# Performance work log

Hardware: AMD Instinct MI355X
Metric: run time of the kernel (lower is better)

## Reference

```python
import jax, jax.numpy as jnp
import numpy as np


def _l2norm(x, axis=-1, eps=1e-12):
    # matches F.normalize(p=2): x / max(||x||, eps)
    n = jnp.sqrt(jnp.sum(x * x, axis=axis, keepdims=True))
    return x / jnp.maximum(n, eps)


def setup_inputs() -> dict:
    key = jax.random.key(0)
    k1, k2 = jax.random.split(key)
    B, D, C = 262144, 256, 1000
    features = jax.random.normal(k1, (B, D), dtype=jnp.float32)
    labels = jax.random.randint(k2, (B,), 0, C, dtype=jnp.int64)
    return {"features": features, "labels": labels, "num_classes": C}


def reference(features, labels, num_classes):
    labels = labels.astype(jnp.int32)
    f = _l2norm(features, axis=1)  # (B, D)
    # per-class scatter-mean (classes with zero samples contribute no loss terms)
    sums = jax.ops.segment_sum(f, labels, num_segments=num_classes)      # (C, D)
    counts = jax.ops.segment_sum(jnp.ones((f.shape[0],), f.dtype), labels,
                                 num_segments=num_classes)               # (C,)
    protos = sums / jnp.maximum(counts, 1.0)[:, None]
    protos = _l2norm(protos, axis=1)                                     # (C, D)
    # cosine distance of each sample to its own class prototype
    p = protos[labels]                                                   # (B, D)
    dist = 1.0 - jnp.sum(f * p, axis=1)                                  # (B,)
    B = f.shape[0]
    return jnp.sum(dist) / jnp.maximum(B, 1)
```

## Files before the change

kernel.cpp:

```cpp
#include <hip/hip_runtime.h>


#define DIM 256
#define NB 64
#define SSB 2048

typedef float fx4 __attribute__((ext_vector_type(4)));

__global__ __launch_bounds__(256) void k_hist(const int* __restrict__ labels,
                                              int* __restrict__ hist,
                                              float* __restrict__ sums,
                                              int B, int C) {
  extern __shared__ int s_h[];
  const int tid = threadIdx.x;
  for (int i = blockIdx.x * 256 + tid; i < C * DIM; i += NB * 256)
    sums[i] = 0.f;
  for (int c = tid; c < C; c += 256) s_h[c] = 0;
  __syncthreads();
  const int chunk = (B + NB - 1) / NB;
  const int r0 = blockIdx.x * chunk;
  const int r1 = min(B, r0 + chunk);
  for (int i = r0 + tid; i < r1; i += 256) atomicAdd(&s_h[labels[i]], 1);
  __syncthreads();
  int* dst = hist + (size_t)blockIdx.x * C;
  for (int c = tid; c < C; c += 256) dst[c] = s_h[c];
}

__global__ __launch_bounds__(1024) void k_scan(int* __restrict__ hist,
                                               float* __restrict__ out, int C) {
  __shared__ int s[2][1024];
  const int tid = threadIdx.x;
  if (tid == 0) out[0] = 0.f;
  int total = 0;
  if (tid < C) {
    int run = 0;
    for (int b = 0; b < NB; ++b) {
      int* p = hist + (size_t)b * C + tid;
      const int h = *p;
      *p = run;
      run += h;
    }
    total = run;
  }
  int cur = 0;
  s[0][tid] = total;
  __syncthreads();
  for (int d = 1; d < 1024; d <<= 1) {
    const int v = s[cur][tid] + (tid >= d ? s[cur][tid - d] : 0);
    s[1 - cur][tid] = v;
    __syncthreads();
    cur ^= 1;
  }
  const int exoff = s[cur][tid] - total;
  if (tid < C)
    for (int b = 0; b < NB; ++b) hist[(size_t)b * C + tid] += exoff;
}

__global__ __launch_bounds__(256) void k_permute(const int* __restrict__ labels,
                                                 const int* __restrict__ bases,
                                                 int2* __restrict__ pr,
                                                 int B, int C) {
  extern __shared__ int s_cur[];
  const int tid = threadIdx.x;
  const int* bp = bases + (size_t)blockIdx.x * C;
  for (int c = tid; c < C; c += 256) s_cur[c] = bp[c];
  __syncthreads();
  const int chunk = (B + NB - 1) / NB;
  const int r0 = blockIdx.x * chunk;
  const int r1 = min(B, r0 + chunk);
  for (int i = r0 + tid; i < r1; i += 256) {
    const int l = labels[i];
    const int pos = atomicAdd(&s_cur[l], 1);
    pr[pos] = make_int2(i, l);
  }
}

__device__ __forceinline__ void flush_acc(float* __restrict__ sums, int c,
                                          const fx4& a, int lane) {
  float* dst = sums + (size_t)c * DIM + lane * 4;
  atomicAdd(dst + 0, a.x);
  atomicAdd(dst + 1, a.y);
  atomicAdd(dst + 2, a.z);
  atomicAdd(dst + 3, a.w);
}

__global__ __launch_bounds__(256) void k_segsum(const float* __restrict__ x,
                                                const int2* __restrict__ pr,
                                                float* __restrict__ sums,
                                                int B) {
  const int lane = threadIdx.x & 63;
  const int wid = __builtin_amdgcn_readfirstlane(
      (blockIdx.x << 2) | (threadIdx.x >> 6));
  const int nw = SSB * 4;
  const int per = (B + nw - 1) / nw;
  const int r0 = wid * per;
  const int r1 = min(B, r0 + per);
  if (r0 >= r1) return;

  fx4 acc = {0.f, 0.f, 0.f, 0.f};
  int prev = -1;
  int rb = r0;

  for (; rb + 8 <= r1; rb += 8) {
    int2 e[8];
#pragma unroll
    for (int k = 0; k < 8; ++k) e[k] = pr[rb + k];
    fx4 v[8];
#pragma unroll
    for (int k = 0; k < 8; ++k)
      v[k] = __builtin_nontemporal_load(
          (const fx4*)(x + (size_t)e[k].x * DIM) + lane);
    float ss[8];
#pragma unroll
    for (int k = 0; k < 8; ++k)
      ss[k] = v[k].x * v[k].x + v[k].y * v[k].y + v[k].z * v[k].z +
              v[k].w * v[k].w;
#pragma unroll
    for (int off = 32; off; off >>= 1) {
#pragma unroll
      for (int k = 0; k < 8; ++k) ss[k] += __shfl_xor(ss[k], off);
    }
#pragma unroll
    for (int k = 0; k < 8; ++k) {
      const float inv = 1.f / fmaxf(sqrtf(ss[k]), 1e-12f);
      const int lab = e[k].y;
      if (lab != prev) {
        if (prev >= 0) flush_acc(sums, prev, acc, lane);
        acc = (fx4){0.f, 0.f, 0.f, 0.f};
        prev = lab;
      }
      acc.x += v[k].x * inv; acc.y += v[k].y * inv;
      acc.z += v[k].z * inv; acc.w += v[k].w * inv;
    }
  }
  for (; rb < r1; ++rb) {
    const int2 e = pr[rb];
    const fx4 v = ((const fx4*)(x + (size_t)e.x * DIM))[lane];
    float ss = v.x * v.x + v.y * v.y + v.z * v.z + v.w * v.w;
#pragma unroll
    for (int off = 32; off; off >>= 1) ss += __shfl_xor(ss, off);
    const float inv = 1.f / fmaxf(sqrtf(ss), 1e-12f);
    if (e.y != prev) {
      if (prev >= 0) flush_acc(sums, prev, acc, lane);
      acc = (fx4){0.f, 0.f, 0.f, 0.f};
      prev = e.y;
    }
    acc.x += v.x * inv; acc.y += v.y * inv;
    acc.z += v.z * inv; acc.w += v.w * inv;
  }
  if (prev >= 0) flush_acc(sums, prev, acc, lane);
}

__global__ __launch_bounds__(256) void k_norm(const float* __restrict__ sums,
                                              float* __restrict__ out, int C) {
  const int wave = threadIdx.x >> 6;
  const int lane = threadIdx.x & 63;
  const int c = blockIdx.x * 4 + wave;
  float term = 0.f;
  if (c < C) {
    const fx4 v = ((const fx4*)(sums + (size_t)c * DIM))[lane];
    float ss = v.x * v.x + v.y * v.y + v.z * v.z + v.w * v.w;
#pragma unroll
    for (int off = 32; off; off >>= 1) ss += __shfl_xor(ss, off);
    term = sqrtf(ss);
  }
  __shared__ float sp[4];
  if (lane == 0) sp[wave] = term;
  __syncthreads();
  if (threadIdx.x == 0) atomicAdd(out, sp[0] + sp[1] + sp[2] + sp[3]);
}

__global__ void k_final(float* __restrict__ out, int B) {
  out[0] = 1.f - out[0] / (float)B;
}

extern "C" void kernel_launch(void* const* d_in, const int* in_sizes, int n_in,
                              void* d_out, int out_size, void* d_ws, size_t ws_size,
                              hipStream_t stream) {
  const float* x      = (const float*)d_in[0];
  const int*   labels = (const int*)d_in[1];
  const int B = in_sizes[1];
  const int C = 1000;

  char* ws = (char*)d_ws;
  int*   hist = (int*)ws;
  size_t off = ((size_t)NB * C * sizeof(int) + 15) & ~(size_t)15;
  int2*  pr   = (int2*)(ws + off);
  off += (size_t)B * sizeof(int2);
  float* sums = (float*)(ws + off);

  const size_t lds_c = (size_t)C * sizeof(int);
  k_hist<<<NB, 256, lds_c, stream>>>(labels, hist, sums, B, C);
  k_scan<<<1, 1024, 0, stream>>>(hist, (float*)d_out, C);
  k_permute<<<NB, 256, lds_c, stream>>>(labels, hist, pr, B, C);
  k_segsum<<<SSB, 256, 0, stream>>>(x, pr, sums, B);
  k_norm<<<(C + 3) / 4, 256, 0, stream>>>(sums, (float*)d_out, C);
  k_final<<<1, 1, 0, stream>>>((float*)d_out, B);
}
```

Baseline: 394.3 us.

## Replace per-block histogram scan with global counts and global-atomic permute

The per-block histogram and per-block base offsets are replaced by one global class count, built with vectorised int4 label loads over 256 blocks. The scan now only produces one cursor per class. The permute kernel uses global atomics on those cursors, which removes the serial 64-block prefix loop in k_scan. The final kernel is folded into k_norm through a last-block-done counter, and a memset is added. Global atomics on 1000 cursors can contend, and they make the order within each class nondeterministic. The int4 load assumes B is divisible by 4 and that labels are int32.

Measured after the change: 427.5 us. +8.4%, slower.

```diff
diff --git a/kernel.cpp b/kernel.cpp
--- a/kernel.cpp
+++ b/kernel.cpp
@@ -2,46 +2,42 @@
 
 
 #define DIM 256
-#define NB 64
+#define NBC 256
 #define SSB 2048
 
 typedef float fx4 __attribute__((ext_vector_type(4)));
 
-__global__ __launch_bounds__(256) void k_hist(const int* __restrict__ labels,
-                                              int* __restrict__ hist,
-                                              float* __restrict__ sums,
-                                              int B, int C) {
-  extern __shared__ int s_h[];
+__global__ __launch_bounds__(256) void k_count(const int4* __restrict__ labels4,
+                                               int* __restrict__ cnt,
+                                               float* __restrict__ sums,
+                                               int B4, int C, int CD) {
+  __shared__ int s_h[1024];
   const int tid = threadIdx.x;
-  for (int i = blockIdx.x * 256 + tid; i < C * DIM; i += NB * 256)
-    sums[i] = 0.f;
-  for (int c = tid; c < C; c += 256) s_h[c] = 0;
+  const int gid = blockIdx.x * 256 + tid;
+  for (int i = gid; i < CD; i += NBC * 256) sums[i] = 0.f;
+  for (int c = tid; c < 1024; c += 256) s_h[c] = 0;
   __syncthreads();
-  const int chunk = (B + NB - 1) / NB;
-  const int r0 = blockIdx.x * chunk;
-  const int r1 = min(B, r0 + chunk);
-  for (int i = r0 + tid; i < r1; i += 256) atomicAdd(&s_h[labels[i]], 1);
+  for (int i = gid; i < B4; i += NBC * 256) {
+    const int4 L = labels4[i];
+    atomicAdd(&s_h[L.x], 1);
+    atomicAdd(&s_h[L.y], 1);
+    atomicAdd(&s_h[L.z], 1);
+    atomicAdd(&s_h[L.w], 1);
+  }
   __syncthreads();
-  int* dst = hist + (size_t)blockIdx.x * C;
-  for (int c = tid; c < C; c += 256) dst[c] = s_h[c];
+  for (int c = tid; c < C; c += 256) {
+    const int v = s_h[c];
+    if (v) atomicAdd(&cnt[c], v);
+  }
 }
 
-__global__ __launch_bounds__(1024) void k_scan(int* __restrict__ hist,
+__global__ __launch_bounds__(1024) void k_scan(const int* __restrict__ cnt,
+                                               int* __restrict__ cursors,
                                                float* __restrict__ out, int C) {
   __shared__ int s[2][1024];
   const int tid = threadIdx.x;
   if (tid == 0) out[0] = 0.f;
-  int total = 0;
-  if (tid < C) {
-    int run = 0;
-    for (int b = 0; b < NB; ++b) {
-      int* p = hist + (size_t)b * C + tid;
-      const int h = *p;
-      *p = run;
-      run += h;
-    }
-    total = run;
-  }
+  const int total = (tid < C) ? cnt[tid] : 0;
   int cur = 0;
   s[0][tid] = total;
   __syncthreads();
@@ -51,26 +47,16 @@
     __syncthreads();
     cur ^= 1;
   }
-  const int exoff = s[cur][tid] - total;
-  if (tid < C)
-    for (int b = 0; b < NB; ++b) hist[(size_t)b * C + tid] += exoff;
+  if (tid < C) cursors[tid] = s[cur][tid] - total;
 }
 
 __global__ __launch_bounds__(256) void k_permute(const int* __restrict__ labels,
-                                                 const int* __restrict__ bases,
-                                                 int2* __restrict__ pr,
-                                                 int B, int C) {
-  extern __shared__ int s_cur[];
-  const int tid = threadIdx.x;
-  const int* bp = bases + (size_t)blockIdx.x * C;
-  for (int c = tid; c < C; c += 256) s_cur[c] = bp[c];
-  __syncthreads();
-  const int chunk = (B + NB - 1) / NB;
-  const int r0 = blockIdx.x * chunk;
-  const int r1 = min(B, r0 + chunk);
-  for (int i = r0 + tid; i < r1; i += 256) {
+                                                 int* __restrict__ cursors,
+                                                 int2* __restrict__ pr, int B) {
+  const int gid = blockIdx.x * 256 + threadIdx.x;
+  for (int i = gid; i < B; i += NBC * 256) {
     const int l = labels[i];
-    const int pos = atomicAdd(&s_cur[l], 1);
+    const int pos = atomicAdd(&cursors[l], 1);
     pr[pos] = make_int2(i, l);
   }
 }
@@ -152,7 +138,9 @@
 }
 
 __global__ __launch_bounds__(256) void k_norm(const float* __restrict__ sums,
-                                              float* __restrict__ out, int C) {
+                                              float* __restrict__ out,
+                                              unsigned* __restrict__ done,
+                                              int C, int B) {
   const int wave = threadIdx.x >> 6;
   const int lane = threadIdx.x & 63;
   const int c = blockIdx.x * 4 + wave;
@@ -167,11 +155,15 @@
   __shared__ float sp[4];
   if (lane == 0) sp[wave] = term;
   __syncthreads();
-  if (threadIdx.x == 0) atomicAdd(out, sp[0] + sp[1] + sp[2] + sp[3]);
-}
-
-__global__ void k_final(float* __restrict__ out, int B) {
-  out[0] = 1.f - out[0] / (float)B;
+  if (threadIdx.x == 0) {
+    atomicAdd(out, sp[0] + sp[1] + sp[2] + sp[3]);
+    __threadfence();
+    const unsigned d = atomicAdd(done, 1u);
+    if (d == gridDim.x - 1) {
+      const float t = atomicAdd(out, 0.f);
+      out[0] = 1.f - t / (float)B;
+    }
+  }
 }
 
 extern "C" void kernel_launch(void* const* d_in, const int* in_sizes, int n_in,
@@ -183,17 +175,21 @@
   const int C = 1000;
 
   char* ws = (char*)d_ws;
-  int*   hist = (int*)ws;
-  size_t off = ((size_t)NB * C * sizeof(int) + 15) & ~(size_t)15;
+  int*      cnt     = (int*)ws;
+  unsigned* done    = (unsigned*)(ws + (size_t)C * sizeof(int));
+  int*      cursors = (int*)(ws + (size_t)(C + 1) * sizeof(int));
+  size_t off = (((size_t)(2 * C + 1) * sizeof(int)) + 15) & ~(size_t)15;
   int2*  pr   = (int2*)(ws + off);
   off += (size_t)B * sizeof(int2);
   float* sums = (float*)(ws + off);
 
-  const size_t lds_c = (size_t)C * sizeof(int);
-  k_hist<<<NB, 256, lds_c, stream>>>(labels, hist, sums, B, C);
-  k_scan<<<1, 1024, 0, stream>>>(hist, (float*)d_out, C);
-  k_permute<<<NB, 256, lds_c, stream>>>(labels, hist, pr, B, C);
+  hipMemsetAsync(cnt, 0, (size_t)(C + 1) * sizeof(int), stream);
+
+  k_count<<<NBC, 256, 0, stream>>>((const int4*)labels, cnt, sums, B / 4, C,
+                                   C * DIM);
+  k_scan<<<1, 1024, 0, stream>>>(cnt, cursors, (float*)d_out, C);
+  k_permute<<<NBC, 256, 0, stream>>>(labels, cursors, pr, B);
   k_segsum<<<SSB, 256, 0, stream>>>(x, pr, sums, B);
-  k_norm<<<(C + 3) / 4, 256, 0, stream>>>(sums, (float*)d_out, C);
-  k_final<<<1, 1, 0, stream>>>((float*)d_out, B);
+  const int nblk = (C + 3) / 4;
+  k_norm<<<nblk, 256, 0, stream>>>(sums, (float*)d_out, done, C, B);
 }
```
